# Performance work log

Measured on AMD Instinct MI355X. Metric: run time of the kernel, lower is better.

Reference implementation:

```python
import jax, jax.numpy as jnp
import numpy as np

K = 3   # num nearest neighbors (init k)
P = 2   # IDW power (init p)


def setup_inputs() -> dict:
    key = jax.random.key(0)
    k1, k2, k3, k4 = jax.random.split(key, 4)
    B, N, M, C = 8, 16384, 1024, 256
    xyz = jax.random.normal(k1, (B, N, 3), dtype=jnp.float32)
    sampled_xyz = jax.random.normal(k2, (B, M, 3), dtype=jnp.float32)
    sampled_features = jax.random.normal(k3, (B, M, C), dtype=jnp.float32)
    masks = jax.random.randint(k4, (B, N), 0, 2, dtype=jnp.int32)
    return {"xyz": xyz, "sampled_xyz": sampled_xyz,
            "sampled_features": sampled_features, "masks": masks}


def reference(xyz, sampled_xyz, sampled_features, masks):
    # xyz: [B,N,3], sampled_xyz: [B,M,3], sampled_features: [B,M,C], masks: [B,N]
    # Squared pairwise distances [B,N,M] (same math as the chunked torch loop).
    delta = xyz[:, :, None, :] - sampled_xyz[:, None, :, :]
    dists = jnp.sum(delta * delta, axis=-1)
    # k smallest distances -> negate and take top-k.
    neg_top, idx = jax.lax.top_k(-dists, K)          # [B,N,K]
    min_dists = jnp.maximum(-neg_top, 1e-10)
    weights = 1.0 / (min_dists ** P + 1e-10)
    weights = weights / jnp.sum(weights, axis=-1, keepdims=True)
    # Gather neighbor features: [B,N,K,C]
    gathered = jax.vmap(lambda f, i: f[i])(sampled_features, idx)
    interpolated = jnp.sum(gathered * weights[..., None], axis=2)  # [B,N,C]
    # Invalid (masked-out) rows stay zero, matching the padded scatter.
    valid = (masks != 0).astype(interpolated.dtype)
    return interpolated * valid[..., None]
```

## Files before the change

### kernel.cpp

```cpp
#include <hip/hip_runtime.h>

constexpr int B = 8;
constexpr int N = 16384;
constexpr int M = 1024;
constexpr int C = 256;
constexpr int PTS = 64;
constexpr int QW  = 4;

__global__ __launch_bounds__(256, 8) void upsample_idw_kernel(
    const float* __restrict__ xyz,
    const float* __restrict__ sxyz,
    const float* __restrict__ feats,
    const int*   __restrict__ masks,
    float*       __restrict__ out)
{
    const int tid = threadIdx.x;
    const int w   = tid >> 6;
    const int l   = tid & 63;
    const int blk = blockIdx.x;
    const int b     = blk >> 8;
    const int nbase = (blk & 255) << 6;

    __shared__ char s_mem[M * 3 * 4];
    float* s_cand = (float*)s_mem;
    unsigned long long (*s_key)[QW][3] = (unsigned long long (*)[QW][3])s_mem;
    __shared__ float s_w[PTS][3];
    __shared__ int   s_j[PTS][4];

    {
        const float4* src = (const float4*)(sxyz + (size_t)b * (M * 3));
        float4* dst = (float4*)s_mem;
        #pragma unroll
        for (int i = 0; i < 3; ++i)
            dst[tid + 256 * i] = src[tid + 256 * i];
    }

    const int n = nbase + l;
    const float* xp = xyz + ((size_t)b * N + n) * 3;
    const float x = xp[0], y = xp[1], z = xp[2];
    __syncthreads();

    const float* cp = s_cand + w * (256 * 3);

    float d0 = __builtin_inff(), d1 = __builtin_inff(), d2 = __builtin_inff();
    int   i0 = 0, i1 = 0, i2 = 0;

    #pragma unroll 4
    for (int m = 0; m < 256; ++m) {
        const float sx = cp[3 * m + 0];
        const float sy = cp[3 * m + 1];
        const float sz = cp[3 * m + 2];
        const float dx = __fsub_rn(x, sx);
        const float dy = __fsub_rn(y, sy);
        const float dz = __fsub_rn(z, sz);
        const float d  = __fadd_rn(__fadd_rn(__fmul_rn(dx, dx), __fmul_rn(dy, dy)),
                                   __fmul_rn(dz, dz));
        const bool lt0 = d < d0, lt1 = d < d1, lt2 = d < d2;
        i2 = lt1 ? i1 : (lt2 ? m : i2);
        i1 = lt0 ? i0 : (lt1 ? m : i1);
        i0 = lt0 ? m  : i0;
        const float nd2 = __builtin_amdgcn_fmed3f(d1, d2, d);
        const float nd1 = __builtin_amdgcn_fmed3f(d0, d1, d);
        d2 = nd2;
        d1 = nd1;
        d0 = fminf(d0, d);
    }
    __syncthreads();

    const unsigned base = (unsigned)(w * 256);
    s_key[l][w][0] = ((unsigned long long)__float_as_uint(d0) << 32) | (base + (unsigned)i0);
    s_key[l][w][1] = ((unsigned long long)__float_as_uint(d1) << 32) | (base + (unsigned)i1);
    s_key[l][w][2] = ((unsigned long long)__float_as_uint(d2) << 32) | (base + (unsigned)i2);
    __syncthreads();

    if (tid < PTS) {
        unsigned long long k0 = ~0ULL, k1 = ~0ULL, k2 = ~0ULL;
        #pragma unroll
        for (int q = 0; q < QW; ++q) {
            #pragma unroll
            for (int s = 0; s < 3; ++s) {
                const unsigned long long k = s_key[tid][q][s];
                const bool lt0 = k < k0, lt1 = k < k1, lt2 = k < k2;
                k2 = lt1 ? k1 : (lt2 ? k : k2);
                k1 = lt0 ? k0 : (lt1 ? k : k1);
                k0 = lt0 ? k  : k0;
            }
        }
        const float e0 = __uint_as_float((unsigned)(k0 >> 32));
        const float e1 = __uint_as_float((unsigned)(k1 >> 32));
        const float e2 = __uint_as_float((unsigned)(k2 >> 32));
        const float m0 = fmaxf(e0, 1e-10f);
        const float m1 = fmaxf(e1, 1e-10f);
        const float m2 = fmaxf(e2, 1e-10f);
        float w0 = 1.0f / (m0 * m0 + 1e-10f);
        float w1 = 1.0f / (m1 * m1 + 1e-10f);
        float w2 = 1.0f / (m2 * m2 + 1e-10f);
        const int valid = masks[(size_t)b * N + nbase + tid];
        const float scale = valid ? (1.0f / (w0 + w1 + w2)) : 0.0f;
        s_w[tid][0] = w0 * scale;
        s_w[tid][1] = w1 * scale;
        s_w[tid][2] = w2 * scale;
        s_j[tid][0] = (int)(unsigned)k0;
        s_j[tid][1] = (int)(unsigned)k1;
        s_j[tid][2] = (int)(unsigned)k2;
        s_j[tid][3] = valid;
    }
    __syncthreads();

    const int pq = tid >> 6;
    const int cq = tid & 63;
    const float4* Fb4 = (const float4*)(feats + (size_t)b * (M * C));
    float4* op4 = (float4*)(out + (((size_t)b * N + nbase) * C));

    for (int p0 = 0; p0 < PTS; p0 += 4) {
        const int p = p0 + pq;
        const int vld = __builtin_amdgcn_readfirstlane(s_j[p][3]);
        float4 acc = make_float4(0.f, 0.f, 0.f, 0.f);
        if (vld) {
            const int j0 = __builtin_amdgcn_readfirstlane(s_j[p][0]);
            const int j1 = __builtin_amdgcn_readfirstlane(s_j[p][1]);
            const int j2 = __builtin_amdgcn_readfirstlane(s_j[p][2]);
            const float w0 = __uint_as_float(
                __builtin_amdgcn_readfirstlane((int)__float_as_uint(s_w[p][0])));
            const float w1 = __uint_as_float(
                __builtin_amdgcn_readfirstlane((int)__float_as_uint(s_w[p][1])));
            const float w2 = __uint_as_float(
                __builtin_amdgcn_readfirstlane((int)__float_as_uint(s_w[p][2])));
            const float4 f0 = Fb4[j0 * 64 + cq];
            const float4 f1 = Fb4[j1 * 64 + cq];
            const float4 f2 = Fb4[j2 * 64 + cq];
            acc.x = fmaf(w2, f2.x, fmaf(w1, f1.x, w0 * f0.x));
            acc.y = fmaf(w2, f2.y, fmaf(w1, f1.y, w0 * f0.y));
            acc.z = fmaf(w2, f2.z, fmaf(w1, f1.z, w0 * f0.z));
            acc.w = fmaf(w2, f2.w, fmaf(w1, f1.w, w0 * f0.w));
        }
        op4[p * 64 + cq] = acc;
    }
}

extern "C" void kernel_launch(void* const* d_in, const int* in_sizes, int n_in,
                              void* d_out, int out_size, void* d_ws, size_t ws_size,
                              hipStream_t stream) {
    const float* xyz   = (const float*)d_in[0];
    const float* sxyz  = (const float*)d_in[1];
    const float* feats = (const float*)d_in[2];
    const int*   masks = (const int*)d_in[3];
    float*       out   = (float*)d_out;

    dim3 grid(B * N / PTS);
    dim3 block(256);
    hipLaunchKernelGGL(upsample_idw_kernel, grid, block, 0, stream,
                       xyz, sxyz, feats, masks, out);
}
```

Baseline: 72.97 us.

## Stream candidate coordinates via scalar loads instead of LDS staging

Candidate coordinates are no longer staged in shared memory. Each wave now loads 48-float chunks straight into scalar registers with inline s_load_dwordx16, so the coordinates are wave-uniform SGPR operands and the per-candidate LDS reads and the first barrier go away. Blocks are also remapped to interleave batches (b = blk & 7), and shared memory shrinks to just the key buffer. This should raise occupancy. The cost is a full lgkmcnt wait on every chunk with no overlap between loads and compute, plus heavy SGPR pressure from the inline asm.

```diff
diff --git a/kernel.cpp b/kernel.cpp
--- a/kernel.cpp
+++ b/kernel.cpp
@@ -6,6 +6,8 @@
 constexpr int C = 256;
 constexpr int PTS = 64;
 constexpr int QW  = 4;
+
+typedef float vf16 __attribute__((ext_vector_type(16)));
 
 __global__ __launch_bounds__(256, 8) void upsample_idw_kernel(
     const float* __restrict__ xyz,
@@ -18,54 +20,53 @@
     const int w   = tid >> 6;
     const int l   = tid & 63;
     const int blk = blockIdx.x;
-    const int b     = blk >> 8;
-    const int nbase = (blk & 255) << 6;
+    const int b     = blk & 7;
+    const int nbase = (blk >> 3) << 6;
 
-    __shared__ char s_mem[M * 3 * 4];
-    float* s_cand = (float*)s_mem;
-    unsigned long long (*s_key)[QW][3] = (unsigned long long (*)[QW][3])s_mem;
+    __shared__ unsigned long long s_key[PTS][QW][3];
     __shared__ float s_w[PTS][3];
     __shared__ int   s_j[PTS][4];
 
-    {
-        const float4* src = (const float4*)(sxyz + (size_t)b * (M * 3));
-        float4* dst = (float4*)s_mem;
-        #pragma unroll
-        for (int i = 0; i < 3; ++i)
-            dst[tid + 256 * i] = src[tid + 256 * i];
-    }
+    const float* xp = xyz + ((size_t)b * N + nbase + l) * 3;
+    const float x = xp[0], y = xp[1], z = xp[2];
 
-    const int n = nbase + l;
-    const float* xp = xyz + ((size_t)b * N + n) * 3;
-    const float x = xp[0], y = xp[1], z = xp[2];
-    __syncthreads();
-
-    const float* cp = s_cand + w * (256 * 3);
+    const float* bbase = sxyz + (size_t)b * (M * 3);
+    const int qoff = __builtin_amdgcn_readfirstlane((tid >> 6) * (256 * 12));
 
     float d0 = __builtin_inff(), d1 = __builtin_inff(), d2 = __builtin_inff();
     int   i0 = 0, i1 = 0, i2 = 0;
 
-    #pragma unroll 4
-    for (int m = 0; m < 256; ++m) {
-        const float sx = cp[3 * m + 0];
-        const float sy = cp[3 * m + 1];
-        const float sz = cp[3 * m + 2];
-        const float dx = __fsub_rn(x, sx);
-        const float dy = __fsub_rn(y, sy);
-        const float dz = __fsub_rn(z, sz);
-        const float d  = __fadd_rn(__fadd_rn(__fmul_rn(dx, dx), __fmul_rn(dy, dy)),
-                                   __fmul_rn(dz, dz));
-        const bool lt0 = d < d0, lt1 = d < d1, lt2 = d < d2;
-        i2 = lt1 ? i1 : (lt2 ? m : i2);
-        i1 = lt0 ? i0 : (lt1 ? m : i1);
-        i0 = lt0 ? m  : i0;
-        const float nd2 = __builtin_amdgcn_fmed3f(d1, d2, d);
-        const float nd1 = __builtin_amdgcn_fmed3f(d0, d1, d);
-        d2 = nd2;
-        d1 = nd1;
-        d0 = fminf(d0, d);
+    for (int ch = 0; ch < 16; ++ch) {
+        vf16 ca, cb, cc;
+        const int off = qoff + ch * 192;
+        asm volatile(
+            "s_load_dwordx16 %0, %3, %4\n\t"
+            "s_load_dwordx16 %1, %3, %4 offset:64\n\t"
+            "s_load_dwordx16 %2, %3, %4 offset:128\n\t"
+            "s_waitcnt lgkmcnt(0)"
+            : "=&s"(ca), "=&s"(cb), "=&s"(cc)
+            : "s"(bbase), "s"(off));
+        #pragma unroll
+        for (int j = 0; j < 16; ++j) {
+            const int f0 = 3 * j, f1 = 3 * j + 1, f2 = 3 * j + 2;
+            const float cx = (f0 < 16) ? ca[f0 & 15] : (f0 < 32) ? cb[f0 & 15] : cc[f0 & 15];
+            const float cy = (f1 < 16) ? ca[f1 & 15] : (f1 < 32) ? cb[f1 & 15] : cc[f1 & 15];
+            const float cz = (f2 < 16) ? ca[f2 & 15] : (f2 < 32) ? cb[f2 & 15] : cc[f2 & 15];
+            const float dx = __fsub_rn(cx, x);
+            const float dy = __fsub_rn(cy, y);
+            const float dz = __fsub_rn(cz, z);
+            const float d  = __fadd_rn(__fadd_rn(__fmul_rn(dx, dx), __fmul_rn(dy, dy)),
+                                       __fmul_rn(dz, dz));
+            const int m = ch * 16 + j;
+            const bool lt0 = d < d0, lt1 = d < d1, lt2 = d < d2;
+            i2 = lt1 ? i1 : (lt2 ? m : i2);
+            i1 = lt0 ? i0 : (lt1 ? m : i1);
+            i0 = lt0 ? m  : i0;
+            const float nd2 = __builtin_amdgcn_fmed3f(d1, d2, d);
+            const float nd1 = __builtin_amdgcn_fmed3f(d0, d1, d);
+            d2 = nd2; d1 = nd1; d0 = fminf(d0, d);
+        }
     }
-    __syncthreads();
 
     const unsigned base = (unsigned)(w * 256);
     s_key[l][w][0] = ((unsigned long long)__float_as_uint(d0) << 32) | (base + (unsigned)i0);
```

Result: faster. 66.24 us (-9.2%).
